# Kernel optimization log

Hardware: AMD Instinct MI355X
Metric: run time of the kernel (lower is better)

## Reference

```python
import jax, jax.numpy as jnp
import numpy as np

B, S, E, D, H = 4, 1024, 1024, 1024, 16   # batch, dec_seq, enc_seq, d_model, n_heads
DH = D // H
DFF = 4096
EPS = 1e-5


def setup_inputs() -> dict:
    key = jax.random.key(0)
    ks = jax.random.split(key, 16)
    w = lambda k, shp: (jax.random.normal(k, shp, dtype=jnp.float32) * 0.02)
    return {
        "x": jax.random.normal(ks[0], (B, S, D), dtype=jnp.float32),
        "enc_x": jax.random.normal(ks[1], (B, E, D), dtype=jnp.float32),
        # masked self-attn (fused qkv)
        "w_qkv": w(ks[2], (D, 3 * D)), "b_qkv": jnp.zeros((3 * D,), jnp.float32),
        "w_sa_o": w(ks[3], (D, D)), "b_sa_o": jnp.zeros((D,), jnp.float32),
        # cross-attn
        "w_q": w(ks[4], (D, D)), "b_q": jnp.zeros((D,), jnp.float32),
        "w_k": w(ks[5], (D, D)), "b_k": jnp.zeros((D,), jnp.float32),
        "w_v": w(ks[6], (D, D)), "b_v": jnp.zeros((D,), jnp.float32),
        "w_ca_o": w(ks[7], (D, D)), "b_ca_o": jnp.zeros((D,), jnp.float32),
        # ffn
        "w1": w(ks[8], (D, DFF)), "b1": jnp.zeros((DFF,), jnp.float32),
        "w2": w(ks[9], (DFF, D)), "b2": jnp.zeros((D,), jnp.float32),
        # layernorms
        "g1": jnp.ones((D,), jnp.float32), "be1": jnp.zeros((D,), jnp.float32),
        "g2": jnp.ones((D,), jnp.float32), "be2": jnp.zeros((D,), jnp.float32),
        "g3": jnp.ones((D,), jnp.float32), "be3": jnp.zeros((D,), jnp.float32),
    }


def _layernorm(x, g, b):
    mean = jnp.mean(x, axis=-1, keepdims=True)
    var = jnp.mean(jnp.square(x - mean), axis=-1, keepdims=True)  # unbiased=False
    return g * (x - mean) / jnp.sqrt(var + EPS) + b


def _masked_self_attn(x, w_qkv, b_qkv, w_o, b_o):
    b, s, d = x.shape
    qkv = x @ w_qkv + b_qkv                            # [b,s,3D]
    # Faithful to torch: view as [b,s,H,3*DH] then chunk last dim (interleaved per-head).
    qkv = qkv.reshape(b, s, H, 3 * DH).transpose(0, 2, 1, 3)   # [b,H,s,3DH]
    q, k, v = jnp.split(qkv, 3, axis=-1)               # each [b,H,s,DH]
    scores = jnp.einsum('bhqd,bhkd->bhqk', q, k) / jnp.sqrt(jnp.float32(DH))
    mask = jnp.triu(jnp.ones((s, s), dtype=bool), k=1)
    scores = jnp.where(mask, -jnp.inf, scores)
    attn = jax.nn.softmax(scores, axis=-1)
    out = jnp.einsum('bhqk,bhkd->bhqd', attn, v)       # [b,H,s,DH]
    out = out.transpose(0, 2, 1, 3).reshape(b, s, d)
    return out @ w_o + b_o


def _cross_attn(dec_x, enc_x, w_q, b_q, w_k, b_k, w_v, b_v, w_o, b_o):
    b, sq, d = dec_x.shape
    sk = enc_x.shape[1]
    q = (dec_x @ w_q + b_q).reshape(b, sq, H, DH).transpose(0, 2, 1, 3)
    k = (enc_x @ w_k + b_k).reshape(b, sk, H, DH).transpose(0, 2, 1, 3)
    v = (enc_x @ w_v + b_v).reshape(b, sk, H, DH).transpose(0, 2, 1, 3)
    scores = jnp.einsum('bhqd,bhkd->bhqk', q, k) / jnp.sqrt(jnp.float32(DH))
    attn = jax.nn.softmax(scores, axis=-1)
    out = jnp.einsum('bhqk,bhkd->bhqd', attn, v).transpose(0, 2, 1, 3).reshape(b, sq, d)
    return out @ w_o + b_o


def reference(x, enc_x, w_qkv, b_qkv, w_sa_o, b_sa_o,
              w_q, b_q, w_k, b_k, w_v, b_v, w_ca_o, b_ca_o,
              w1, b1, w2, b2, g1, be1, g2, be2, g3, be3):
    h = _layernorm(x + _masked_self_attn(x, w_qkv, b_qkv, w_sa_o, b_sa_o), g1, be1)
    h = _layernorm(h + _cross_attn(h, enc_x, w_q, b_q, w_k, b_k, w_v, b_v, w_ca_o, b_ca_o), g2, be2)
    ffn = jax.nn.gelu(h @ w1 + b1, approximate=False) @ w2 + b2  # torch F.gelu default = exact
    return _layernorm(h + ffn, g3, be3)
```

## Files before the change

kernel.cpp:

```cpp
#include <hip/hip_runtime.h>

#define BB 4
#define SS 1024
#define DD 1024
#define HH 16
#define DHH 64
#define DFF 4096
#define MROWS 4096
#define NEG_BIG (-1e30f)
#define LOG2E 1.4426950408889634f
#define SCL_L2E 0.1803368801111244f

typedef float  f32x4  __attribute__((ext_vector_type(4)));
typedef __bf16 bf16x8 __attribute__((ext_vector_type(8)));
typedef __bf16 bf16x4 __attribute__((ext_vector_type(4)));

#define DEV __device__ __forceinline__

DEV void glds16(const __bf16* g, __bf16* l) {
  __builtin_amdgcn_global_load_lds((__attribute__((address_space(1))) void*)(g),
                                   (__attribute__((address_space(3))) void*)(l),
                                   16, 0, 0);
}

DEV float sanit(float v) {
  return fminf(fmaxf(v, -1e30f), 1e30f);
}

__global__ __launch_bounds__(256) void cvt_bf16(const float* __restrict__ src,
                                                __bf16* __restrict__ dst)
{
  const int idx = blockIdx.x * 256 + threadIdx.x;
  const f32x4 v = ((const f32x4*)src)[idx];
  bf16x4 o;
#pragma unroll
  for (int i = 0; i < 4; i++) o[i] = (__bf16)v[i];
  ((bf16x4*)dst)[idx] = o;
}

__global__ __launch_bounds__(256) void wtrans(const float* __restrict__ src,
                                              __bf16* __restrict__ dst,
                                              int K, int N)
{
  __shared__ float t[64][65];
  const int k0 = blockIdx.y * 64, n0 = blockIdx.x * 64;
  const int c = threadIdx.x & 63, r0 = threadIdx.x >> 6;
#pragma unroll
  for (int i = 0; i < 16; i++) {
    const int r = r0 * 16 + i;
    t[r][c] = src[(size_t)(k0 + r) * N + n0 + c];
  }
  __syncthreads();
#pragma unroll
  for (int i = 0; i < 16; i++) {
    const int r = r0 * 16 + i;
    dst[(size_t)(n0 + r) * K + k0 + c] = (__bf16)t[c][r];
  }
}

__global__ __launch_bounds__(256) void vtrans(const __bf16* __restrict__ src,
                                              int stride, int colMul, int colAdd,
                                              __bf16* __restrict__ dst)
{
  __shared__ __bf16 t[64][66];
  const int bh = blockIdx.y, b = bh >> 4, h = bh & 15;
  const int s0 = blockIdx.x * 64;
  const int c = threadIdx.x & 63, r0 = threadIdx.x >> 6;
  const __bf16* sp = src + (size_t)(b * SS) * stride + h * colMul + colAdd;
#pragma unroll
  for (int i = 0; i < 16; i++) {
    const int s = r0 * 16 + i;
    t[s][c] = sp[(size_t)(s0 + s) * stride + c];
  }
  __syncthreads();
  __bf16* dp = dst + (size_t)bh * 64 * 1024;
#pragma unroll
  for (int i = 0; i < 16; i++) {
    const int d = r0 * 16 + i;
    dp[(size_t)d * 1024 + s0 + c] = t[c][d];
  }
}

template<int MODE>
__global__ __launch_bounds__(256) void gemm_bt(
    const __bf16* __restrict__ A, const __bf16* __restrict__ Bt,
    const float* __restrict__ bias, void* __restrict__ Cout,
    int N, int K)
{
  __shared__ __align__(16) __bf16 As[128 * 32];
  __shared__ __align__(16) __bf16 Bs[128 * 32];

  const int bm = blockIdx.y * 128, bn = blockIdx.x * 128;
  const int tid = threadIdx.x, wid = tid >> 6, lane = tid & 63;
  const int quad = lane >> 4, ln = lane & 15;

  const __bf16* gA = A  + (size_t)(bm + wid * 32 + (lane >> 2)) * K + (lane & 3) * 8;
  const __bf16* gB = Bt + (size_t)(bn + wid * 32 + (lane >> 2)) * K + (lane & 3) * 8;
  __bf16* lA = As + (wid * 32) * 32;
  __bf16* lB = Bs + (wid * 32) * 32;

  f32x4 acc[4][4];
#pragma unroll
  for (int i = 0; i < 4; i++)
#pragma unroll
    for (int j = 0; j < 4; j++) acc[i][j] = (f32x4){0.f, 0.f, 0.f, 0.f};

  const int wr = (wid >> 1) * 64, wc = (wid & 1) * 64;

  for (int k0 = 0; k0 < K; k0 += 32) {
    glds16(gA + k0,           lA);
    glds16(gA + 16 * K + k0,  lA + 16 * 32);
    glds16(gB + k0,           lB);
    glds16(gB + 16 * K + k0,  lB + 16 * 32);
    __syncthreads();

    bf16x8 af[4], bfr[4];
#pragma unroll
    for (int i = 0; i < 4; i++)
      af[i] = *(const bf16x8*)(As + (wr + i * 16 + ln) * 32 + quad * 8);
#pragma unroll
    for (int j = 0; j < 4; j++)
      bfr[j] = *(const bf16x8*)(Bs + (wc + j * 16 + ln) * 32 + quad * 8);
#pragma unroll
    for (int i = 0; i < 4; i++)
#pragma unroll
      for (int j = 0; j < 4; j++)
        acc[i][j] = __builtin_amdgcn_mfma_f32_16x16x32_bf16(af[i], bfr[j], acc[i][j], 0, 0, 0);
    __syncthreads();
  }

#pragma unroll
  for (int j = 0; j < 4; j++) {
    const int col = bn + wc + j * 16 + ln;
    const float bv = bias[col];
#pragma unroll
    for (int i = 0; i < 4; i++) {
#pragma unroll
      for (int r = 0; r < 4; r++) {
        const int row = bm + wr + i * 16 + quad * 4 + r;
        float v = sanit(acc[i][j][r] + bv);
        if (MODE == 1) v = 0.5f * v * (1.f + erff(v * 0.70710678118654752f));
        if (MODE == 3 && (col % 192) < 64) v *= SCL_L2E;
        if (MODE == 2) ((float*)Cout)[(size_t)row * N + col] = v;
        else           ((__bf16*)Cout)[(size_t)row * N + col] = (__bf16)v;
      }
    }
  }
}

template<int MODE>
__global__ __launch_bounds__(256) void gemm_bt64(
    const __bf16* __restrict__ A, const __bf16* __restrict__ Bt,
    const float* __restrict__ bias, void* __restrict__ Cout,
    int N, int K)
{
  __shared__ __align__(16) __bf16 As[128 * 32];
  __shared__ __align__(16) __bf16 Bs[64 * 32];

  const int bm = blockIdx.y * 128, bn = blockIdx.x * 64;
  const int tid = threadIdx.x, wid = tid >> 6, lane = tid & 63;
  const int quad = lane >> 4, ln = lane & 15;

  const __bf16* gA = A  + (size_t)(bm + wid * 32 + (lane >> 2)) * K + (lane & 3) * 8;
  const __bf16* gB = Bt + (size_t)(bn + wid * 16 + (lane >> 2)) * K + (lane & 3) * 8;
  __bf16* lA = As + (wid * 32) * 32;
  __bf16* lB = Bs + (wid * 16) * 32;

  f32x4 acc[4][2];
#pragma unroll
  for (int i = 0; i < 4; i++)
#pragma unroll
    for (int j = 0; j < 2; j++) acc[i][j] = (f32x4){0.f, 0.f, 0.f, 0.f};

  const int wr = (wid >> 1) * 64, wc = (wid & 1) * 32;

  for (int k0 = 0; k0 < K; k0 += 32) {
    glds16(gA + k0,           lA);
    glds16(gA + 16 * K + k0,  lA + 16 * 32);
    glds16(gB + k0,           lB);
    __syncthreads();

    bf16x8 af[4], bfr[2];
#pragma unroll
    for (int i = 0; i < 4; i++)
      af[i] = *(const bf16x8*)(As + (wr + i * 16 + ln) * 32 + quad * 8);
#pragma unroll
    for (int j = 0; j < 2; j++)
      bfr[j] = *(const bf16x8*)(Bs + (wc + j * 16 + ln) * 32 + quad * 8);
#pragma unroll
    for (int i = 0; i < 4; i++)
#pragma unroll
      for (int j = 0; j < 2; j++)
        acc[i][j] = __builtin_amdgcn_mfma_f32_16x16x32_bf16(af[i], bfr[j], acc[i][j], 0, 0, 0);
    __syncthreads();
  }

#pragma unroll
  for (int j = 0; j < 2; j++) {
    const int col = bn + wc + j * 16 + ln;
    const float bv = bias[col];
#pragma unroll
    for (int i = 0; i < 4; i++) {
#pragma unroll
      for (int r = 0; r < 4; r++) {
        const int row = bm + wr + i * 16 + quad * 4 + r;
        float v = sanit(acc[i][j][r] + bv);
        if (MODE == 3) v *= SCL_L2E;
        if (MODE == 2) ((float*)Cout)[(size_t)row * N + col] = v;
        else           ((__bf16*)Cout)[(size_t)row * N + col] = (__bf16)v;
      }
    }
  }
}

__global__ __launch_bounds__(256) void attn(
    const __bf16* __restrict__ qp, int qStride, int qMul, int qAdd,
    const __bf16* __restrict__ kp, int kStride, int kMul, int kAdd,
    const __bf16* __restrict__ vt, __bf16* __restrict__ outp, int causal)
{
  __shared__ __align__(16) __bf16 Kt[2][64 * 64];
  __shared__ __align__(16) __bf16 Vt[2][64 * 64];
  __shared__ __align__(16) __bf16 ptl[4][32 * 64];

  const int id = blockIdx.x;
  const int bh = ((id >> 6) << 3) | (id & 7);
  const int qblk = (id >> 3) & 7;
  const int b = bh >> 4, h = bh & 15;
  const int tid = threadIdx.x, wid = tid >> 6, lane = tid & 63;
  const int quad = lane >> 4, ln = lane & 15;
  const int qbase = qblk * 128;
  const int rowb0 = qbase + wid * 32;
  const int rowTop = rowb0 + 31;

  bf16x8 aq[2][2];
#pragma unroll
  for (int rf = 0; rf < 2; ++rf) {
    const __bf16* qr = qp + (size_t)(b * SS + rowb0 + rf * 16 + ln) * qStride
                          + h * qMul + qAdd;
#pragma unroll
    for (int ks = 0; ks < 2; ++ks)
      aq[rf][ks] = *(const bf16x8*)(qr + ks * 32 + quad * 8);
  }

  f32x4 acc[2][4];
#pragma unroll
  for (int rf = 0; rf < 2; ++rf)
#pragma unroll
    for (int nb = 0; nb < 4; ++nb) acc[rf][nb] = (f32x4){0.f, 0.f, 0.f, 0.f};
  float l_r[2][4] = {{0.f,0.f,0.f,0.f},{0.f,0.f,0.f,0.f}};

  const __bf16* kbase = kp + (size_t)(b * SS) * kStride + h * kMul + kAdd;
  const __bf16* vtb = vt + (size_t)bh * 64 * 1024;
  __bf16* ptw = ptl[wid];

  const int kvEnd = causal ? (qbase + 128) : SS;
  const int nT = kvEnd >> 6;

  const int sr = wid * 16 + (lane >> 3);
  const int sq = lane & 7;

#pragma unroll
  for (int p = 0; p < 2; ++p) {
    const int r = sr + p * 8;
    const int qs = (sq ^ (r & 7)) * 8;
    glds16(kbase + (size_t)r * kStride + qs, Kt[0] + (wid * 2 + p) * 512);
    glds16(vtb + (size_t)r * 1024 + qs,      Vt[0] + (wid * 2 + p) * 512);
  }

  for (int t = 0; t < nT; ++t) {
    const int cur = t & 1;
    const int kv0 = t * 64;

    if (t + 1 < nT) {
      const int kn = kv0 + 64;
#pragma unroll
      for (int p = 0; p < 2; ++p) {
        const int r = sr + p * 8;
        const int qs = (sq ^ (r & 7)) * 8;
        glds16(kbase + (size_t)(kn + r) * kStride + qs, Kt[cur ^ 1] + (wid * 2 + p) * 512);
        glds16(vtb + (size_t)r * 1024 + kn + qs,        Vt[cur ^ 1] + (wid * 2 + p) * 512);
      }
      __asm__ volatile("s_waitcnt vmcnt(4)" ::: "memory");
    } else {
      __asm__ volatile("s_waitcnt vmcnt(0)" ::: "memory");
    }
    __builtin_amdgcn_sched_barrier(0);
    __builtin_amdgcn_s_barrier();
    __asm__ volatile("" ::: "memory");
    __builtin_amdgcn_sched_barrier(0);

    if (!causal || kv0 <= rowTop) {
      const __bf16* kt = Kt[cur];
      const __bf16* vv = Vt[cur];

      f32x4 sc[2][4];
      {
        bf16x8 kf[4][2];
#pragma unroll
        for (int c = 0; c < 4; ++c) {
          const int row = c * 16 + ln;
#pragma unroll
          for (int ks = 0; ks < 2; ++ks)
            kf[c][ks] = *(const bf16x8*)(kt + row * 64 + (((ks * 4 + quad) ^ (ln & 7)) * 8));
        }
#pragma unroll
        for (int rf = 0; rf < 2; ++rf)
#pragma unroll
          for (int c = 0; c < 4; ++c) {
            f32x4 s_ = (f32x4){0.f, 0.f, 0.f, 0.f};
            s_ = __builtin_amdgcn_mfma_f32_16x16x32_bf16(aq[rf][0], kf[c][0], s_, 0, 0, 0);
            s_ = __builtin_amdgcn_mfma_f32_16x16x32_bf16(aq[rf][1], kf[c][1], s_, 0, 0, 0);
            sc[rf][c] = s_;
          }
      }

#pragma unroll
      for (int rf = 0; rf < 2; ++rf) {
        const bool doMask = causal && (kv0 + 63 > rowb0 + rf * 16);
#pragma unroll
        for (int r = 0; r < 4; ++r) {
          const int rowg = rowb0 + rf * 16 + quad * 4 + r;
          float p[4];
#pragma unroll
          for (int c = 0; c < 4; ++c) {
            float e = sc[rf][c][r];
            if (doMask && (kv0 + c * 16 + ln > rowg)) e = NEG_BIG;
            p[c] = exp2f(e);
          }
          l_r[rf][r] += (p[0] + p[1]) + (p[2] + p[3]);
          const int m = rf * 16 + quad * 4 + r;
          __bf16* pr = ptw + m * 64;
#pragma unroll
          for (int c = 0; c < 4; ++c) {
            const int col = c * 16 + ln;
            pr[(((col >> 3) ^ (m & 7)) << 3) + (col & 7)] = (__bf16)p[c];
          }
        }
      }
      __asm__ volatile("s_waitcnt lgkmcnt(0)" ::: "memory");
      __builtin_amdgcn_sched_barrier(0);

      {
        bf16x8 pa[2][2];
#pragma unroll
        for (int rf = 0; rf < 2; ++rf) {
          const int m = rf * 16 + ln;
#pragma unroll
          for (int ks = 0; ks < 2; ++ks)
            pa[rf][ks] = *(const bf16x8*)(ptw + m * 64 + (((ks * 4 + quad) ^ (m & 7)) * 8));
        }
#pragma unroll
        for (int nb = 0; nb < 4; ++nb) {
          const int vrow = nb * 16 + ln;
          const bf16x8 vf0 = *(const bf16x8*)(vv + vrow * 64 + (((quad)     ^ (ln & 7)) * 8));
          const bf16x8 vf1 = *(const bf16x8*)(vv + vrow * 64 + (((4 + quad) ^ (ln & 7)) * 8));
#pragma unroll
          for (int rf = 0; rf < 2; ++rf) {
            acc[rf][nb] = __builtin_amdgcn_mfma_f32_16x16x32_bf16(pa[rf][0], vf0, acc[rf][nb], 0, 0, 0);
            acc[rf][nb] = __builtin_amdgcn_mfma_f32_16x16x32_bf16(pa[rf][1], vf1, acc[rf][nb], 0, 0, 0);
          }
        }
      }
    }

    __asm__ volatile("" ::: "memory");
    __builtin_amdgcn_sched_barrier(0);
    __builtin_amdgcn_s_barrier();
  }

#pragma unroll
  for (int rf = 0; rf < 2; ++rf) {
#pragma unroll
    for (int r = 0; r < 4; ++r) {
      float l = l_r[rf][r];
#pragma unroll
      for (int off = 1; off < 16; off <<= 1) l += __shfl_xor(l, off, 64);
      const float inv = 1.f / fmaxf(l, 1e-30f);
      const int rowg = rowb0 + rf * 16 + quad * 4 + r;
      __bf16* op = outp + (size_t)(b * SS + rowg) * DD + h * 64;
#pragma unroll
      for (int nb = 0; nb < 4; ++nb)
        op[nb * 16 + ln] = (__bf16)sanit(acc[rf][nb][r] * inv);
    }
  }
}

__global__ __launch_bounds__(256) void ln_k(
    const float* __restrict__ residf, const float* __restrict__ proj,
    const float* __restrict__ g, const float* __restrict__ be,
    float* __restrict__ outf, __bf16* __restrict__ outb)
{
  const int row = blockIdx.x, tid = threadIdx.x;
  const f32x4 pb = ((const f32x4*)(proj   + (size_t)row * 1024))[tid];
  const f32x4 rb = ((const f32x4*)(residf + (size_t)row * 1024))[tid];
  f32x4 x;
#pragma unroll
  for (int i = 0; i < 4; i++)
    x[i] = fminf(fmaxf(pb[i] + rb[i], -1e15f), 1e15f);
  float s  = x[0] + x[1] + x[2] + x[3];
  float ss = x[0]*x[0] + x[1]*x[1] + x[2]*x[2] + x[3]*x[3];
#pragma unroll
  for (int off = 1; off < 64; off <<= 1) {
    s  += __shfl_xor(s,  off, 64);
    ss += __shfl_xor(ss, off, 64);
  }
  __shared__ float sm[8];
  if ((tid & 63) == 0) { sm[tid >> 6] = s; sm[4 + (tid >> 6)] = ss; }
  __syncthreads();
  s  = sm[0] + sm[1] + sm[2] + sm[3];
  ss = sm[4] + sm[5] + sm[6] + sm[7];
  const float mean = s * (1.f / 1024.f);
  const float var  = fmaxf(ss * (1.f / 1024.f) - mean * mean, 0.f);
  const float rstd = rsqrtf(var + 1e-5f);
  const int c = tid * 4;
  f32x4 o;
#pragma unroll
  for (int i = 0; i < 4; i++)
    o[i] = g[c + i] * ((x[i] - mean) * rstd) + be[c + i];
  if (outf) ((f32x4*)(outf + (size_t)row * 1024))[tid] = o;
  if (outb) {
    bf16x4 ob;
#pragma unroll
    for (int i = 0; i < 4; i++) ob[i] = (__bf16)o[i];
    ((bf16x4*)(outb + (size_t)row * 1024))[tid] = ob;
  }
}

extern "C" void kernel_launch(void* const* d_in, const int* in_sizes, int n_in,
                              void* d_out, int out_size, void* d_ws, size_t ws_size,
                              hipStream_t stream)
{
  const float* x      = (const float*)d_in[0];
  const float* enc    = (const float*)d_in[1];
  const float* w_qkv  = (const float*)d_in[2];
  const float* b_qkv  = (const float*)d_in[3];
  const float* w_sa_o = (const float*)d_in[4];
  const float* b_sa_o = (const float*)d_in[5];
  const float* w_q    = (const float*)d_in[6];
  const float* b_q    = (const float*)d_in[7];
  const float* w_k    = (const float*)d_in[8];
  const float* b_k    = (const float*)d_in[9];
  const float* w_v    = (const float*)d_in[10];
  const float* b_v    = (const float*)d_in[11];
  const float* w_ca_o = (const float*)d_in[12];
  const float* b_ca_o = (const float*)d_in[13];
  const float* w1     = (const float*)d_in[14];
  const float* b1     = (const float*)d_in[15];
  const float* w2     = (const float*)d_in[16];
  const float* b2     = (const float*)d_in[17];
  const float* g1     = (const float*)d_in[18];
  const float* be1    = (const float*)d_in[19];
  const float* g2     = (const float*)d_in[20];
  const float* be2    = (const float*)d_in[21];
  const float* g3     = (const float*)d_in[22];
  const float* be3    = (const float*)d_in[23];

  const size_t MB = 1024 * 1024;
  char* base = (char*)d_ws;
  __bf16* wqkvT = (__bf16*)(base + 0 * MB);
  __bf16* wsaoT = (__bf16*)(base + 6 * MB);
  __bf16* wqT   = (__bf16*)(base + 8 * MB);
  __bf16* wkT   = (__bf16*)(base + 10 * MB);
  __bf16* wvT   = (__bf16*)(base + 12 * MB);
  __bf16* wcaoT = (__bf16*)(base + 14 * MB);
  __bf16* w1T   = (__bf16*)(base + 0 * MB);
  __bf16* w2T   = (__bf16*)(base + 8 * MB);
  __bf16* xb    = (__bf16*)(base + 16 * MB);
  __bf16* encb  = (__bf16*)(base + 24 * MB);
  __bf16* qkv   = (__bf16*)(base + 32 * MB);
  __bf16* vt    = (__bf16*)(base + 56 * MB);
  __bf16* mid   = (__bf16*)(base + 32 * MB);
  __bf16* attnb = (__bf16*)(base + 64 * MB);
  float*  proj  = (float*) (base + 72 * MB);
  float*  h1f   = (float*) (base + 88 * MB);
  __bf16* h1b   = (__bf16*)(base + 104 * MB);
  float*  h2f   = (float*) (base + 112 * MB);
  __bf16* h2b   = (__bf16*)(base + 128 * MB);
  __bf16* qb = qkv;
  __bf16* kb = qkv + (size_t)MROWS * 1024;
  __bf16* vb = qkv + (size_t)MROWS * 2048;

  cvt_bf16<<<4096, 256, 0, stream>>>(x,   xb);
  cvt_bf16<<<4096, 256, 0, stream>>>(enc, encb);
  wtrans<<<dim3(48, 16), 256, 0, stream>>>(w_qkv,  wqkvT, 1024, 3072);
  wtrans<<<dim3(16, 16), 256, 0, stream>>>(w_sa_o, wsaoT, 1024, 1024);
  wtrans<<<dim3(16, 16), 256, 0, stream>>>(w_q,    wqT,   1024, 1024);
  wtrans<<<dim3(16, 16), 256, 0, stream>>>(w_k,    wkT,   1024, 1024);
  wtrans<<<dim3(16, 16), 256, 0, stream>>>(w_v,    wvT,   1024, 1024);
  wtrans<<<dim3(16, 16), 256, 0, stream>>>(w_ca_o, wcaoT, 1024, 1024);

  gemm_bt<3><<<dim3(24, 32), 256, 0, stream>>>(xb, wqkvT, b_qkv, qkv, 3072, 1024);
  vtrans<<<dim3(16, 64), 256, 0, stream>>>(qkv, 3072, 192, 128, vt);
  attn<<<512, 256, 0, stream>>>(qkv, 3072, 192, 0,
                                qkv, 3072, 192, 64, vt, attnb, 1);
  gemm_bt64<2><<<dim3(16, 32), 256, 0, stream>>>(attnb, wsaoT, b_sa_o, proj, 1024, 1024);
  ln_k<<<4096, 256, 0, stream>>>(x, proj, g1, be1, h1f, h1b);

  gemm_bt64<3><<<dim3(16, 32), 256, 0, stream>>>(h1b, wqT, b_q, qb, 1024, 1024);
  gemm_bt64<0><<<dim3(16, 32), 256, 0, stream>>>(encb, wkT, b_k, kb, 1024, 1024);
  gemm_bt64<0><<<dim3(16, 32), 256, 0, stream>>>(encb, wvT, b_v, vb, 1024, 1024);
  vtrans<<<dim3(16, 64), 256, 0, stream>>>(vb, 1024, 64, 0, vt);
  attn<<<512, 256, 0, stream>>>(qb, 1024, 64, 0,
                                kb, 1024, 64, 0, vt, attnb, 0);
  gemm_bt64<2><<<dim3(16, 32), 256, 0, stream>>>(attnb, wcaoT, b_ca_o, proj, 1024, 1024);
  ln_k<<<4096, 256, 0, stream>>>(h1f, proj, g2, be2, h2f, h2b);

  wtrans<<<dim3(64, 16), 256, 0, stream>>>(w1, w1T, 1024, 4096);
  wtrans<<<dim3(16, 64), 256, 0, stream>>>(w2, w2T, 4096, 1024);
  gemm_bt<1><<<dim3(32, 32), 256, 0, stream>>>(h2b, w1T, b1, mid, 4096, 1024);
  gemm_bt64<2><<<dim3(16, 32), 256, 0, stream>>>(mid, w2T, b2, proj, 1024, 4096);
  ln_k<<<4096, 256, 0, stream>>>(h2f, proj, g3, be3, (float*)d_out, nullptr);

  (void)in_sizes; (void)n_in; (void)out_size; (void)ws_size;
}
```

Measured before the change: 606.7 us.

## Double-buffer GEMM LDS tiles and use polynomial erf approximation for GELU

New measurement: 597.7 us. No clear change (-1.5%).

```diff
diff --git a/kernel.cpp b/kernel.cpp
--- a/kernel.cpp
+++ b/kernel.cpp
@@ -27,6 +27,16 @@
   return fminf(fmaxf(v, -1e30f), 1e30f);
 }
 
+DEV float gelu_f(float v) {
+  const float z  = fabsf(v) * 0.70710678118654752f;
+  const float t  = __builtin_amdgcn_rcpf(1.f + 0.3275911f * z);
+  float poly = ((((1.061405429f * t - 1.453152027f) * t + 1.421413741f) * t
+                 - 0.284496736f) * t + 0.254829592f) * t;
+  float er = 1.f - poly * __expf(-z * z);
+  er = copysignf(er, v);
+  return 0.5f * v * (1.f + er);
+}
+
 __global__ __launch_bounds__(256) void cvt_bf16(const float* __restrict__ src,
                                                 __bf16* __restrict__ dst)
 {
@@ -87,8 +97,8 @@
     const float* __restrict__ bias, void* __restrict__ Cout,
     int N, int K)
 {
-  __shared__ __align__(16) __bf16 As[128 * 32];
-  __shared__ __align__(16) __bf16 Bs[128 * 32];
+  __shared__ __align__(16) __bf16 As[2][128 * 32];
+  __shared__ __align__(16) __bf16 Bs[2][128 * 32];
 
   const int bm = blockIdx.y * 128, bn = blockIdx.x * 128;
   const int tid = threadIdx.x, wid = tid >> 6, lane = tid & 63;
@@ -96,8 +106,7 @@
 
   const __bf16* gA = A  + (size_t)(bm + wid * 32 + (lane >> 2)) * K + (lane & 3) * 8;
   const __bf16* gB = Bt + (size_t)(bn + wid * 32 + (lane >> 2)) * K + (lane & 3) * 8;
-  __bf16* lA = As + (wid * 32) * 32;
-  __bf16* lB = Bs + (wid * 32) * 32;
+  const int soff = (wid * 32) * 32;
 
   f32x4 acc[4][4];
 #pragma unroll
@@ -107,27 +116,42 @@
 
   const int wr = (wid >> 1) * 64, wc = (wid & 1) * 64;
 
-  for (int k0 = 0; k0 < K; k0 += 32) {
-    glds16(gA + k0,           lA);
-    glds16(gA + 16 * K + k0,  lA + 16 * 32);
-    glds16(gB + k0,           lB);
-    glds16(gB + 16 * K + k0,  lB + 16 * 32);
+#define G_STAGE(buf, kt) do {                                     \
+    const int k0_ = (kt) * 32;                                    \
+    glds16(gA + k0_,          &As[buf][soff]);                    \
+    glds16(gA + 16 * K + k0_, &As[buf][soff + 16 * 32]);          \
+    glds16(gB + k0_,          &Bs[buf][soff]);                    \
+    glds16(gB + 16 * K + k0_, &Bs[buf][soff + 16 * 32]);          \
+  } while (0)
+
+#define G_COMP(buf) do {                                                    \
+    bf16x8 af[4], bfr[4];                                                   \
+    _Pragma("unroll")                                                       \
+    for (int i = 0; i < 4; i++)                                             \
+      af[i] = *(const bf16x8*)(&As[buf][(wr + i * 16 + ln) * 32 + quad * 8]); \
+    _Pragma("unroll")                                                       \
+    for (int j = 0; j < 4; j++)                                             \
+      bfr[j] = *(const bf16x8*)(&Bs[buf][(wc + j * 16 + ln) * 32 + quad * 8]); \
+    _Pragma("unroll")                                                       \
+    for (int i = 0; i < 4; i++)                                             \
+      _Pragma("unroll")                                                     \
+      for (int j = 0; j < 4; j++)                                           \
+        acc[i][j] = __builtin_amdgcn_mfma_f32_16x16x32_bf16(af[i], bfr[j], acc[i][j], 0, 0, 0); \
+  } while (0)
+
+  const int nk = K >> 5;
+  G_STAGE(0, 0);
+  __syncthreads();
+  for (int kt = 0; kt < nk; kt += 2) {
+    G_STAGE(1, kt + 1);
+    G_COMP(0);
     __syncthreads();
-
-    bf16x8 af[4], bfr[4];
-#pragma unroll
-    for (int i = 0; i < 4; i++)
-      af[i] = *(const bf16x8*)(As + (wr + i * 16 + ln) * 32 + quad * 8);
-#pragma unroll
-    for (int j = 0; j < 4; j++)
-      bfr[j] = *(const bf16x8*)(Bs + (wc + j * 16 + ln) * 32 + quad * 8);
-#pragma unroll
-    for (int i = 0; i < 4; i++)
-#pragma unroll
-      for (int j = 0; j < 4; j++)
-        acc[i][j] = __builtin_amdgcn_mfma_f32_16x16x32_bf16(af[i], bfr[j], acc[i][j], 0, 0, 0);
+    if (kt + 2 < nk) G_STAGE(0, kt + 2);
+    G_COMP(1);
     __syncthreads();
   }
+#undef G_STAGE
+#undef G_COMP
 
 #pragma unroll
   for (int j = 0; j < 4; j++) {
@@ -139,7 +163,7 @@
       for (int r = 0; r < 4; r++) {
         const int row = bm + wr + i * 16 + quad * 4 + r;
         float v = sanit(acc[i][j][r] + bv);
-        if (MODE == 1) v = 0.5f * v * (1.f + erff(v * 0.70710678118654752f));
+        if (MODE == 1) v = gelu_f(v);
         if (MODE == 3 && (col % 192) < 64) v *= SCL_L2E;
         if (MODE == 2) ((float*)Cout)[(size_t)row * N + col] = v;
         else           ((__bf16*)Cout)[(size_t)row * N + col] = (__bf16)v;
@@ -154,8 +178,8 @@
     const float* __restrict__ bias, void* __restrict__ Cout,
     int N, int K)
 {
-  __shared__ __align__(16) __bf16 As[128 * 32];
-  __shared__ __align__(16) __bf16 Bs[64 * 32];
+  __shared__ __align__(16) __bf16 As[2][128 * 32];
+  __shared__ __align__(16) __bf16 Bs[2][64 * 32];
 
   const int bm = blockIdx.y * 128, bn = blockIdx.x * 64;
   const int tid = threadIdx.x, wid = tid >> 6, lane = tid & 63;
@@ -163,8 +187,8 @@
 
   const __bf16* gA = A  + (size_t)(bm + wid * 32 + (lane >> 2)) * K + (lane & 3) * 8;
   const __bf16* gB = Bt + (size_t)(bn + wid * 16 + (lane >> 2)) * K + (lane & 3) * 8;
-  __bf16* lA = As + (wid * 32) * 32;
-  __bf16* lB = Bs + (wid * 16) * 32;
+  const int aoff = (wid * 32) * 32;
+  const int boff = (wid * 16) * 32;
 
   f32x4 acc[4][2];
 #pragma unroll
@@ -174,26 +198,41 @@
 
   const int wr = (wid >> 1) * 64, wc = (wid & 1) * 32;
 
-  for (int k0 = 0; k0 < K; k0 += 32) {
-    glds16(gA + k0,           lA);
-    glds16(gA + 16 * K + k0,  lA + 16 * 32);
-    glds16(gB + k0,           lB);
+#define G_STAGE(buf, kt) do {                                     \
+    const int k0_ = (kt) * 32;                                    \
+    glds16(gA + k0_,          &As[buf][aoff]);                    \
+    glds16(gA + 16 * K + k0_, &As[buf][aoff + 16 * 32]);          \
+    glds16(gB + k0_,          &Bs[buf][boff]);                    \
+  } while (0)
+
+#define G_COMP(buf) do {                                                    \
+    bf16x8 af[4], bfr[2];                                                   \
+    _Pragma("unroll")                                                       \
+    for (int i = 0; i < 4; i++)                                             \
+      af[i] = *(const bf16x8*)(&As[buf][(wr + i * 16 + ln) * 32 + quad * 8]); \
+    _Pragma("unroll")                                                       \
+    for (int j = 0; j < 2; j++)                                             \
+      bfr[j] = *(const bf16x8*)(&Bs[buf][(wc + j * 16 + ln) * 32 + quad * 8]); \
+    _Pragma("unroll")                                                       \
+    for (int i = 0; i < 4; i++)                                             \
+      _Pragma("unroll")                                                     \
+      for (int j = 0; j < 2; j++)                                           \
+        acc[i][j] = __builtin_amdgcn_mfma_f32_16x16x32_bf16(af[i], bfr[j], acc[i][j], 0, 0, 0); \
+  } while (0)
+
+  const int nk = K >> 5;
+  G_STAGE(0, 0);
+  __syncthreads();
+  for (int kt = 0; kt < nk; kt += 2) {
+    G_STAGE(1, kt + 1);
+    G_COMP(0);
     __syncthreads();
-
-    bf16x8 af[4], bfr[2];
-#pragma unroll
-    for (int i = 0; i < 4; i++)
-      af[i] = *(const bf16x8*)(As + (wr + i * 16 + ln) * 32 + quad * 8);
-#pragma unroll
-    for (int j = 0; j < 2; j++)
-      bfr[j] = *(const bf16x8*)(Bs + (wc + j * 16 + ln) * 32 + quad * 8);
-#pragma unroll
-    for (int i = 0; i < 4; i++)
-#pragma unroll
-      for (int j = 0; j < 2; j++)
-        acc[i][j] = __builtin_amdgcn_mfma_f32_16x16x32_bf16(af[i], bfr[j], acc[i][j], 0, 0, 0);
+    if (kt + 2 < nk) G_STAGE(0, kt + 2);
+    G_COMP(1);
     __syncthreads();
   }
+#undef G_STAGE
+#undef G_COMP
 
 #pragma unroll
   for (int j = 0; j < 2; j++) {
```
